# Optimization experiments

Hardware: AMD Instinct MI355X
Metric: run time of the kernel (lower is better)

Reference implementation:

```python
import jax, jax.numpy as jnp
import numpy as np

L = 2        # num_layers
H = 512      # hidden_size
IN = 32      # input_size = output_size + 24
OUT = 8      # output_size
B = 512      # batch
S = 128      # encoder seq_len
F = 48       # future_len
TF = 24      # time-feature dim


def setup_inputs() -> dict:
    key = jax.random.key(0)
    ks = jax.random.split(key, 14)
    def rn(k, shape, s=0.05):
        return jax.random.normal(k, shape, dtype=jnp.float32) * s
    return {
        "x": rn(ks[0], (S, B, IN), 1.0),
        "future_time": rn(ks[1], (F - 1, B, TF), 1.0),
        "h0": rn(ks[2], (L, 1, H), 1.0),
        "c0": rn(ks[3], (L, 1, H), 1.0),
        # PyTorch nn.LSTM weights: gate order (i, f, g, o), rows of 4H
        "w_ih0": rn(ks[4], (4 * H, IN)),
        "w_hh0": rn(ks[5], (4 * H, H)),
        "b_ih0": rn(ks[6], (4 * H,)),
        "b_hh0": rn(ks[7], (4 * H,)),
        "w_ih1": rn(ks[8], (4 * H, H)),
        "w_hh1": rn(ks[9], (4 * H, H)),
        "b_ih1": rn(ks[10], (4 * H,)),
        "b_hh1": rn(ks[11], (4 * H,)),
        "fc_w": rn(ks[12], (OUT, H)),
        "fc_b": rn(ks[13], (OUT,)),
    }


def _cell(x, h, c, w_ih, w_hh, b):
    # PyTorch LSTMCell math, gate order i,f,g,o
    gates = x @ w_ih.T + h @ w_hh.T + b  # [B, 4H]
    i, f, g, o = jnp.split(gates, 4, axis=-1)
    c2 = jax.nn.sigmoid(f) * c + jax.nn.sigmoid(i) * jnp.tanh(g)
    h2 = jax.nn.sigmoid(o) * jnp.tanh(c2)
    return h2, c2


def reference(x, future_time, h0, c0,
              w_ih0, w_hh0, b_ih0, b_hh0,
              w_ih1, w_hh1, b_ih1, b_hh1,
              fc_w, fc_b):
    batch = x.shape[1]
    params = [(w_ih0, w_hh0, b_ih0 + b_hh0),
              (w_ih1, w_hh1, b_ih1 + b_hh1)]
    h_init = jnp.broadcast_to(h0, (L, batch, H))
    c_init = jnp.broadcast_to(c0, (L, batch, H))

    def multi_step(carry, x_t):
        hs, cs = carry
        new_h, new_c = [], []
        inp = x_t
        for l, (wi, wh, b) in enumerate(params):
            h2, c2 = _cell(inp, hs[l], cs[l], wi, wh, b)
            new_h.append(h2)
            new_c.append(c2)
            inp = h2
        return (jnp.stack(new_h), jnp.stack(new_c)), inp

    # encoder pass over the conditioning sequence
    (hs, cs), outs = jax.lax.scan(multi_step, (h_init, c_init), x)
    y0 = outs[-1] @ fc_w.T + fc_b  # [B, OUT], first prediction

    def dec_step(carry, t_feat):
        hs, cs, y = carry
        x_t = jnp.concatenate([y, t_feat], axis=-1)  # [B, OUT+TF] == [B, IN]
        (hs2, cs2), h_top = multi_step((hs, cs), x_t)
        y2 = h_top @ fc_w.T + fc_b
        return (hs2, cs2, y2), y2

    _, ys = jax.lax.scan(dec_step, (hs, cs, y0), future_time)
    return jnp.concatenate([y0[None], ys], axis=0)  # [future_len, B, OUT]
```

## Files before the change

### kernel.cpp

```cpp
#include <hip/hip_runtime.h>


typedef __attribute__((ext_vector_type(8))) short bf16x8;
typedef __attribute__((ext_vector_type(16))) float f32x16;

#define MFMA32(a, b, c) __builtin_amdgcn_mfma_f32_32x32x16_bf16((a), (b), (c), 0, 0, 0)
#define DEV static __device__ __forceinline__

constexpr int kSeq = 128;
constexpr int kT = 175;
constexpr int kRB = 65536;

constexpr size_t kWsHbuf = 0;
constexpr size_t kWsYacc = 2ull * 2 * 8 * kRB;
constexpr size_t kWsFlag = kWsYacc + 2ull * 512 * 8 * 4;
constexpr size_t kWsRc   = kWsFlag + 2ull * 8 * 32 * 64;
constexpr size_t kWsEnd  = kWsRc + 2ull * 8 * 64;
constexpr size_t kWsZeroBegin = kWsYacc;
constexpr size_t kWsZeroSize  = kWsEnd - kWsYacc;

DEV unsigned short f2bf(float f) {
  unsigned u = __float_as_uint(f);
  u += 0x7fffu + ((u >> 16) & 1u);
  return (unsigned short)(u >> 16);
}
DEV float bf2f(unsigned short s) { return __uint_as_float(((unsigned)s) << 16); }
DEV float sigf(float v) { return 1.0f / (1.0f + __expf(-v)); }
DEV float tanhf_(float v) { float e = __expf(2.0f * v); return 1.0f - 2.0f / (e + 1.0f); }
DEV f32x16 zero16() {
  f32x16 z;
#pragma unroll
  for (int i = 0; i < 16; ++i) z[i] = 0.0f;
  return z;
}
DEV bf16x8 pack8(const float* p) {
  float4 a = *(const float4*)p;
  float4 b = *(const float4*)(p + 4);
  bf16x8 r;
  r[0] = (short)f2bf(a.x); r[1] = (short)f2bf(a.y);
  r[2] = (short)f2bf(a.z); r[3] = (short)f2bf(a.w);
  r[4] = (short)f2bf(b.x); r[5] = (short)f2bf(b.y);
  r[6] = (short)f2bf(b.z); r[7] = (short)f2bf(b.w);
  return r;
}

DEV unsigned ald(const unsigned* p) {
  return __hip_atomic_load(p, __ATOMIC_RELAXED, __HIP_MEMORY_SCOPE_AGENT);
}
DEV void ast(unsigned* p, unsigned v) {
  __hip_atomic_store(p, v, __ATOMIC_RELAXED, __HIP_MEMORY_SCOPE_AGENT);
}
DEV unsigned long long ald64(const unsigned long long* p) {
  return __hip_atomic_load(p, __ATOMIC_RELAXED, __HIP_MEMORY_SCOPE_AGENT);
}
DEV void ast64(unsigned long long* p, unsigned long long v) {
  __hip_atomic_store(p, v, __ATOMIC_RELAXED, __HIP_MEMORY_SCOPE_AGENT);
}
DEV float aldf(const float* p) {
  return __hip_atomic_load(p, __ATOMIC_RELAXED, __HIP_MEMORY_SCOPE_AGENT);
}
DEV void astf(float* p, float v) {
  __hip_atomic_store(p, v, __ATOMIC_RELAXED, __HIP_MEMORY_SCOPE_AGENT);
}
DEV void relwait() {
  __atomic_signal_fence(__ATOMIC_SEQ_CST);
  __builtin_amdgcn_s_waitcnt(0);
  __atomic_signal_fence(__ATOMIC_SEQ_CST);
}
DEV bool pollw(const unsigned* slot, unsigned thr) {
  for (int it = 0; it < (1 << 22); ++it) {
    const unsigned v = ald(slot);
    if (__ballot(v < thr) == 0ull) {
      __atomic_signal_fence(__ATOMIC_ACQUIRE);
      return true;
    }
    __builtin_amdgcn_s_sleep(1);
  }
  return false;
}

#define PARTS_WRITE(accv, ms_, ns_)                                           \
  { const int gate_ = (ns_)*2 + gbit;                                         \
    _Pragma("unroll") for (int rg = 0; rg < 16; ++rg) {                       \
      const int r_ = (ms_)*32 + (rg & 3) + 4 * hi5 + 8 * (rg >> 2);           \
      partsB[((kw * 4 + gate_) * 64 + r_) * 17 + l15] = f2bf((accv)[rg]);     \
    } }

__global__ __launch_bounds__(256, 2) void lstm_persist(
    const float* __restrict__ x, const float* __restrict__ ft,
    const float* __restrict__ h0in, const float* __restrict__ c0in,
    const float* __restrict__ wih0, const float* __restrict__ whh0,
    const float* __restrict__ bih0, const float* __restrict__ bhh0,
    const float* __restrict__ wih1, const float* __restrict__ whh1,
    const float* __restrict__ bih1, const float* __restrict__ bhh1,
    const float* __restrict__ fcw, const float* __restrict__ fcb,
    float* __restrict__ out, char* __restrict__ ws) {
  __shared__ __attribute__((aligned(16))) unsigned short partsB[16 * 64 * 17];
  __shared__ __attribute__((aligned(16))) unsigned short xin[64 * 40];
  __shared__ __attribute__((aligned(16))) unsigned short hloc[64 * 24];
  __shared__ float biasl[4][16];
  __shared__ float fcwl[8][16];
  __shared__ unsigned bflag;

  const int bid = blockIdx.x;
  const int layer = bid >> 8;
  const int idx = bid & 255;
  const int bc = idx & 7;
  const int hc = idx >> 3;
  const int b0 = bc * 64;
  const int u0 = hc * 16;
  const int tid = threadIdx.x;
  const int kw = tid >> 6;
  const int lane = tid & 63;
  const int l31 = lane & 31, l15 = lane & 15, hi5 = lane >> 5, gbit = (lane >> 4) & 1;

  char* hbuf = ws + kWsHbuf;
  float* yacc = (float*)(ws + kWsYacc);
  unsigned* flg = (unsigned*)(ws + kWsFlag);
  unsigned* rc = (unsigned*)(ws + kWsRc);

  auto fslot = [&](int l, int b, int h) { return flg + (((l * 8) + b) * 32 + h) * 16; };
  auto region = [&](int p, int l, int b) -> char* {
    return hbuf + (size_t)(((p * 2) + l) * 8 + b) * kRB;
  };

  bool alive = true;

  bf16x8 wf[2][16];
#pragma unroll
  for (int ns = 0; ns < 2; ++ns) {
    const int gate = ns * 2 + gbit;
    const int wrow = gate * 512 + u0 + l15;
    if (layer) {
#pragma unroll
      for (int m = 0; m < 16; ++m) {
        const int jg = kw + 4 * m;
        const int k0 = jg * 16 + hi5 * 8;
        const float* p = (k0 < 512) ? (wih1 + wrow * 512 + k0)
                                    : (whh1 + wrow * 512 + (k0 - 512));
        wf[ns][m] = pack8(p);
      }
    } else {
#pragma unroll
      for (int m = 0; m < 8; ++m) {
        const int jg = kw + 4 * m;
        wf[ns][m] = pack8(whh0 + wrow * 512 + jg * 16 + hi5 * 8);
      }
      if (kw < 2) wf[ns][8] = pack8(wih0 + wrow * 32 + kw * 16 + hi5 * 8);
    }
  }

  if (tid < 64) {
    const int g = tid >> 4, h = tid & 15;
    const int row = g * 512 + u0 + h;
    biasl[g][h] = layer ? (bih1[row] + bhh1[row]) : (bih0[row] + bhh0[row]);
  }
  if (layer && tid >= 64 && tid < 192) {
    const int t2 = tid - 64;
    fcwl[t2 >> 4][t2 & 15] = fcw[(t2 >> 4) * 512 + u0 + (t2 & 15)];
  }

  const int own_h = tid & 15;
  const int own_r0 = (tid >> 4) * 4;
  float cst[4];
  {
    const float cv = c0in[layer * 512 + u0 + own_h];
    cst[0] = cst[1] = cst[2] = cst[3] = cv;
  }

  {
    char* dst = region(layer ? 0 : 1, layer, bc);
    if (tid < 128) {
      const int r = tid >> 1, half = tid & 1;
      union { unsigned short s[8]; unsigned long long u[2]; } v;
#pragma unroll
      for (int k2 = 0; k2 < 8; ++k2)
        v.s[k2] = f2bf(h0in[layer * 512 + u0 + half * 8 + k2]);
      unsigned long long* dp =
          (unsigned long long*)(dst + ((u0 >> 3) + half) * 1024 + r * 16);
      ast64(dp, v.u[0]); ast64(dp + 1, v.u[1]);
    }
    relwait();
    __syncthreads();
    if (tid == 0) ast(fslot(layer, bc, hc), 1u);
  }

  auto xin_store = [&](int r, int c4, float4 v) {
    const int gx = c4 >> 3, half = (c4 >> 2) & 1;
    uint2 pv;
    pv.x = (unsigned)f2bf(v.x) | ((unsigned)f2bf(v.y) << 16);
    pv.y = (unsigned)f2bf(v.z) | ((unsigned)f2bf(v.w) << 16);
    *(uint2*)&xin[r * 40 + ((gx ^ (r & 3)) << 3) + half * 4] = pv;
  };

  auto cell_update = [&]() {
#pragma unroll
    for (int i = 0; i < 4; ++i) {
      const int r = own_r0 + i;
      float ig = biasl[0][own_h], fg = biasl[1][own_h];
      float gg = biasl[2][own_h], og = biasl[3][own_h];
#pragma unroll
      for (int w2 = 0; w2 < 4; ++w2) {
        ig += bf2f(partsB[((w2 * 4 + 0) * 64 + r) * 17 + own_h]);
        fg += bf2f(partsB[((w2 * 4 + 1) * 64 + r) * 17 + own_h]);
        gg += bf2f(partsB[((w2 * 4 + 2) * 64 + r) * 17 + own_h]);
        og += bf2f(partsB[((w2 * 4 + 3) * 64 + r) * 17 + own_h]);
      }
      const float cv = sigf(fg) * cst[i] + sigf(ig) * tanhf_(gg);
      cst[i] = cv;
      hloc[r * 24 + own_h] = f2bf(sigf(og) * tanhf_(cv));
    }
  };

  auto h_publish = [&](char* dst) {
    if (tid < 128) {
      const int r = tid >> 1, half = tid & 1;
      union { uint4 q; unsigned long long u[2]; } v;
      v.q = *(const uint4*)&hloc[r * 24 + half * 8];
      unsigned long long* dp =
          (unsigned long long*)(dst + ((u0 >> 3) + half) * 1024 + r * 16);
      ast64(dp, v.u[0]); ast64(dp + 1, v.u[1]);
    }
  };

  if (layer == 0) {
    for (int t = 0; t < kT; ++t) {
      if (kw == 0 && alive) {
        const unsigned* slot = (lane < 32)
            ? fslot(0, bc, lane)
            : fslot(1, bc, lane - 32);
        const unsigned thr = (lane < 32)
            ? (unsigned)(t + 1)
            : (unsigned)((t < kSeq) ? t : t + 1);
        alive = pollw(slot, thr);
      }
      __syncthreads();

      if (t < kSeq) {
#pragma unroll
        for (int it = 0; it < 2; ++it) {
          const int u = tid + it * 256;
          const int r = u >> 3, c4 = (u & 7) * 4;
          xin_store(r, c4, *(const float4*)&x[(size_t)(t * 512 + b0 + r) * 32 + c4]);
        }
        __syncthreads();
      } else {
        const int q = (t - 1) & 1;
        if (tid < 128) {
          const int r = tid >> 1, o4 = (tid & 1) * 4;
          const float* yp = &yacc[(size_t)(q * 512 + b0 + r) * 8 + o4];
          float4 v;
          v.x = aldf(yp + 0); v.y = aldf(yp + 1);
          v.z = aldf(yp + 2); v.w = aldf(yp + 3);
          const float4 bb = *(const float4*)&fcb[o4];
          v.x += bb.x; v.y += bb.y; v.z += bb.z; v.w += bb.w;
          if (hc == 0)
            *(float4*)&out[(size_t)((t - kSeq) * 512 + b0 + r) * 8 + o4] = v;
          xin_store(r, o4, v);
        }
        for (int u = tid; u < 384; u += 256) {
          const int r = u / 6, m = u - r * 6;
          xin_store(r, 8 + m * 4,
                    *(const float4*)&ft[(size_t)((t - kSeq) * 512 + b0 + r) * 24 + m * 4]);
        }
        __syncthreads();
        if (tid == 0) {
          const unsigned old = __hip_atomic_fetch_add(rc + (q * 8 + bc) * 16, 1u,
                                                      __ATOMIC_RELAXED,
                                                      __HIP_MEMORY_SCOPE_AGENT);
          bflag = (old == 31u) ? 1u : 0u;
        }
        __syncthreads();
        if (bflag) {
          for (int u = tid; u < 512; u += 256)
            astf(&yacc[(size_t)q * 512 * 8 + (size_t)b0 * 8 + u], 0.0f);
          relwait();
          __syncthreads();
          if (tid == 0) ast(rc + (q * 8 + bc) * 16, 0u);
        }
      }

      f32x16 acc00 = zero16(), acc01 = zero16(), acc10 = zero16(), acc11 = zero16();
      const char* hb0 = region((t - 1) & 1, 0, bc);
      unsigned long long abuf[2][16];
#pragma unroll
      for (int i = 0; i < 4; ++i) {
        const size_t off = (size_t)((2 * (kw + 4 * i) + hi5) * 64 + l31) * 16;
        const unsigned long long* p = (const unsigned long long*)(hb0 + off);
        abuf[0][i * 4 + 0] = ald64(p);
        abuf[0][i * 4 + 1] = ald64(p + 1);
        const unsigned long long* q2 = (const unsigned long long*)(hb0 + off + 512);
        abuf[0][i * 4 + 2] = ald64(q2);
        abuf[0][i * 4 + 3] = ald64(q2 + 1);
      }
#pragma unroll
      for (int g = 0; g < 2; ++g) {
        if (g == 0) {
#pragma unroll
          for (int i = 0; i < 4; ++i) {
            const int m = 4 + i;
            const size_t off = (size_t)((2 * (kw + 4 * m) + hi5) * 64 + l31) * 16;
            const unsigned long long* p = (const unsigned long long*)(hb0 + off);
            abuf[1][i * 4 + 0] = ald64(p);
            abuf[1][i * 4 + 1] = ald64(p + 1);
            const unsigned long long* q2 = (const unsigned long long*)(hb0 + off + 512);
            abuf[1][i * 4 + 2] = ald64(q2);
            abuf[1][i * 4 + 3] = ald64(q2 + 1);
          }
        }
#pragma unroll
        for (int i = 0; i < 4; ++i) {
          const int m = g * 4 + i;
          union { unsigned long long u[2]; bf16x8 v; } a0, a1;
          a0.u[0] = abuf[g][i * 4 + 0]; a0.u[1] = abuf[g][i * 4 + 1];
          a1.u[0] = abuf[g][i * 4 + 2]; a1.u[1] = abuf[g][i * 4 + 3];
          acc00 = MFMA32(a0.v, wf[0][m], acc00);
          acc01 = MFMA32(a0.v, wf[1][m], acc01);
          acc10 = MFMA32(a1.v, wf[0][m], acc10);
          acc11 = MFMA32(a1.v, wf[1][m], acc11);
        }
      }
      if (kw < 2) {
#pragma unroll
        for (int ms = 0; ms < 2; ++ms) {
          const int r = ms * 32 + l31;
          const int gx = kw * 2 + hi5;
          const bf16x8 a = *(const bf16x8*)&xin[r * 40 + ((gx ^ (r & 3)) << 3)];
          if (ms == 0) {
            acc00 = MFMA32(a, wf[0][8], acc00);
            acc01 = MFMA32(a, wf[1][8], acc01);
          } else {
            acc10 = MFMA32(a, wf[0][8], acc10);
            acc11 = MFMA32(a, wf[1][8], acc11);
          }
        }
      }
      PARTS_WRITE(acc00, 0, 0); PARTS_WRITE(acc01, 0, 1);
      PARTS_WRITE(acc10, 1, 0); PARTS_WRITE(acc11, 1, 1);
      __syncthreads();
      cell_update();
      __syncthreads();
      h_publish(region(t & 1, 0, bc));
      relwait();
      __syncthreads();
      if (tid == 0) ast(fslot(0, bc, hc), (unsigned)(t + 2));
    }
    if (hc == 0) {
      if (kw == 0 && alive)
        alive = pollw(fslot(1, bc, lane & 31), (unsigned)(kT + 1));
      __syncthreads();
      for (int u = tid; u < 512; u += 256) {
        const int r = u >> 3, o = u & 7;
        out[(size_t)(47 * 512 + b0 + r) * 8 + o] =
            aldf(&yacc[(size_t)(b0 + r) * 8 + o]) + fcb[o];
      }
    }
  } else {
    for (int t = 0; t < kT; ++t) {
      if (kw == 0 && alive) {
        const unsigned* slot = (lane < 32)
            ? fslot(0, bc, lane)
            : fslot(1, bc, lane - 32);
        const unsigned thr = (lane < 32) ? (unsigned)(t + 2) : (unsigned)(t + 1);
        alive = pollw(slot, thr);
      }
      __syncthreads();

      f32x16 acc00 = zero16(), acc01 = zero16(), acc10 = zero16(), acc11 = zero16();
      const char* hbA = region(t & 1, 0, bc);
      const char* hbB = region(t & 1, 1, bc);
      unsigned long long abuf[2][16];
#pragma unroll
      for (int i = 0; i < 4; ++i) {
        const char* base = hbA;
        const size_t off = (size_t)((2 * (kw + 4 * i) + hi5) * 64 + l31) * 16;
        const unsigned long long* p = (const unsigned long long*)(base + off);
        abuf[0][i * 4 + 0] = ald64(p);
        abuf[0][i * 4 + 1] = ald64(p + 1);
        const unsigned long long* q2 = (const unsigned long long*)(base + off + 512);
        abuf[0][i * 4 + 2] = ald64(q2);
        abuf[0][i * 4 + 3] = ald64(q2 + 1);
      }
#pragma unroll
      for (int g = 0; g < 4; ++g) {
        if (g < 3) {
          const int gn = g + 1;
#pragma unroll
          for (int i = 0; i < 4; ++i) {
            const int m = gn * 4 + i;
            const char* base = (m < 8) ? hbA : hbB;
            const int jl = (kw + 4 * m) & 31;
            const size_t off = (size_t)((2 * jl + hi5) * 64 + l31) * 16;
            const unsigned long long* p = (const unsigned long long*)(base + off);
            abuf[gn & 1][i * 4 + 0] = ald64(p);
            abuf[gn & 1][i * 4 + 1] = ald64(p + 1);
            const unsigned long long* q2 = (const unsigned long long*)(base + off + 512);
            abuf[gn & 1][i * 4 + 2] = ald64(q2);
            abuf[gn & 1][i * 4 + 3] = ald64(q2 + 1);
          }
        }
#pragma unroll
        for (int i = 0; i < 4; ++i) {
          const int m = g * 4 + i;
          union { unsigned long long u[2]; bf16x8 v; } a0, a1;
          a0.u[0] = abuf[g & 1][i * 4 + 0]; a0.u[1] = abuf[g & 1][i * 4 + 1];
          a1.u[0] = abuf[g & 1][i * 4 + 2]; a1.u[1] = abuf[g & 1][i * 4 + 3];
          acc00 = MFMA32(a0.v, wf[0][m], acc00);
          acc01 = MFMA32(a0.v, wf[1][m], acc01);
          acc10 = MFMA32(a1.v, wf[0][m], acc10);
          acc11 = MFMA32(a1.v, wf[1][m], acc11);
        }
      }
      PARTS_WRITE(acc00, 0, 0); PARTS_WRITE(acc01, 0, 1);
      PARTS_WRITE(acc10, 1, 0); PARTS_WRITE(acc11, 1, 1);
      __syncthreads();
      cell_update();
      __syncthreads();
      h_publish(region((t & 1) ^ 1, 1, bc));
      if (t >= kSeq - 1) {
        const int q = t & 1;
#pragma unroll
        for (int rep = 0; rep < 2; ++rep) {
          const int i2 = tid + rep * 256;
          const int r = i2 >> 3, o = i2 & 7;
          float s = 0.0f;
#pragma unroll
          for (int h2 = 0; h2 < 16; ++h2)
            s += bf2f(hloc[r * 24 + h2]) * fcwl[o][h2];
          atomicAdd(&yacc[(size_t)(q * 512 + b0 + r) * 8 + o], s);
        }
      }
      relwait();
      __syncthreads();
      if (tid == 0) ast(fslot(1, bc, hc), (unsigned)(t + 2));
    }
  }
}

extern "C" void kernel_launch(void* const* d_in, const int* in_sizes, int n_in,
                              void* d_out, int out_size, void* d_ws, size_t ws_size,
                              hipStream_t stream) {
  (void)in_sizes; (void)n_in; (void)out_size; (void)ws_size;
  hipMemsetAsync((char*)d_ws + kWsZeroBegin, 0, kWsZeroSize, stream);

  const float* x    = (const float*)d_in[0];
  const float* ft   = (const float*)d_in[1];
  const float* h0in = (const float*)d_in[2];
  const float* c0in = (const float*)d_in[3];
  const float* wih0 = (const float*)d_in[4];
  const float* whh0 = (const float*)d_in[5];
  const float* bih0 = (const float*)d_in[6];
  const float* bhh0 = (const float*)d_in[7];
  const float* wih1 = (const float*)d_in[8];
  const float* whh1 = (const float*)d_in[9];
  const float* bih1 = (const float*)d_in[10];
  const float* bhh1 = (const float*)d_in[11];
  const float* fcw  = (const float*)d_in[12];
  const float* fcb  = (const float*)d_in[13];
  float* out = (float*)d_out;
  char* ws = (char*)d_ws;

  void* args[] = {&x, &ft, &h0in, &c0in, &wih0, &whh0, &bih0, &bhh0,
                  &wih1, &whh1, &bih1, &bhh1, &fcw, &fcb, &out, &ws};
  hipError_t err = hipLaunchCooperativeKernel((void*)lstm_persist, dim3(512),
                                              dim3(256), args, 0, stream);
  if (err != hipSuccess) {
    lstm_persist<<<dim3(512), dim3(256), 0, stream>>>(
        x, ft, h0in, c0in, wih0, whh0, bih0, bhh0,
        wih1, whh1, bih1, bhh1, fcw, fcb, out, ws);
  }
}
```

Baseline: 3.383 ms.

## Compute FC output redundantly in layer-0 blocks and deepen layer-0 h buffering

Drops the atomicAdd-based FC accumulation in layer-1 blocks and the reset-counter protocol. Instead, each layer-0 block computes y = h1·fc_w^T itself with MFMA from the published layer-1 hidden state. Layer-0 h buffers go from double to quadruple buffering, which lets layer 0 run up to a few steps ahead of layer 1 during the encoder phase. Layer-1 loads are also issued three groups ahead. This removes global atomics and an extra barrier round, at the cost of every layer-0 block redundantly reading h1 and doing the small FC matmul.

```diff
diff --git a/kernel.cpp b/kernel.cpp
--- a/kernel.cpp
+++ b/kernel.cpp
@@ -11,13 +11,12 @@
 constexpr int kT = 175;
 constexpr int kRB = 65536;
 
-constexpr size_t kWsHbuf = 0;
-constexpr size_t kWsYacc = 2ull * 2 * 8 * kRB;
-constexpr size_t kWsFlag = kWsYacc + 2ull * 512 * 8 * 4;
-constexpr size_t kWsRc   = kWsFlag + 2ull * 8 * 32 * 64;
-constexpr size_t kWsEnd  = kWsRc + 2ull * 8 * 64;
-constexpr size_t kWsZeroBegin = kWsYacc;
-constexpr size_t kWsZeroSize  = kWsEnd - kWsYacc;
+constexpr size_t kWsH0   = 0;
+constexpr size_t kWsH1   = 4ull * 8 * kRB;
+constexpr size_t kWsFlag = kWsH1 + 2ull * 8 * kRB;
+constexpr size_t kWsEnd  = kWsFlag + 2ull * 8 * 32 * 64;
+constexpr size_t kWsZeroBegin = kWsFlag;
+constexpr size_t kWsZeroSize  = kWsEnd - kWsFlag;
 
 DEV unsigned short f2bf(float f) {
   unsigned u = __float_as_uint(f);
@@ -54,12 +53,6 @@
   return __hip_atomic_load(p, __ATOMIC_RELAXED, __HIP_MEMORY_SCOPE_AGENT);
 }
 DEV void ast64(unsigned long long* p, unsigned long long v) {
-  __hip_atomic_store(p, v, __ATOMIC_RELAXED, __HIP_MEMORY_SCOPE_AGENT);
-}
-DEV float aldf(const float* p) {
-  return __hip_atomic_load(p, __ATOMIC_RELAXED, __HIP_MEMORY_SCOPE_AGENT);
-}
-DEV void astf(float* p, float v) {
   __hip_atomic_store(p, v, __ATOMIC_RELAXED, __HIP_MEMORY_SCOPE_AGENT);
 }
 DEV void relwait() {
@@ -99,8 +92,6 @@
   __shared__ __attribute__((aligned(16))) unsigned short xin[64 * 40];
   __shared__ __attribute__((aligned(16))) unsigned short hloc[64 * 24];
   __shared__ float biasl[4][16];
-  __shared__ float fcwl[8][16];
-  __shared__ unsigned bflag;
 
   const int bid = blockIdx.x;
   const int layer = bid >> 8;
@@ -114,14 +105,13 @@
   const int lane = tid & 63;
   const int l31 = lane & 31, l15 = lane & 15, hi5 = lane >> 5, gbit = (lane >> 4) & 1;
 
-  char* hbuf = ws + kWsHbuf;
-  float* yacc = (float*)(ws + kWsYacc);
   unsigned* flg = (unsigned*)(ws + kWsFlag);
-  unsigned* rc = (unsigned*)(ws + kWsRc);
-
   auto fslot = [&](int l, int b, int h) { return flg + (((l * 8) + b) * 32 + h) * 16; };
-  auto region = [&](int p, int l, int b) -> char* {
-    return hbuf + (size_t)(((p * 2) + l) * 8 + b) * kRB;
+  auto region0 = [&](int d, int b) -> char* {
+    return ws + kWsH0 + (size_t)(d * 8 + b) * kRB;
+  };
+  auto region1 = [&](int p, int b) -> char* {
+    return ws + kWsH1 + (size_t)(p * 8 + b) * kRB;
   };
 
   bool alive = true;
@@ -155,10 +145,6 @@
     const int row = g * 512 + u0 + h;
     biasl[g][h] = layer ? (bih1[row] + bhh1[row]) : (bih0[row] + bhh0[row]);
   }
-  if (layer && tid >= 64 && tid < 192) {
-    const int t2 = tid - 64;
-    fcwl[t2 >> 4][t2 & 15] = fcw[(t2 >> 4) * 512 + u0 + (t2 & 15)];
-  }
 
   const int own_h = tid & 15;
   const int own_r0 = (tid >> 4) * 4;
@@ -169,7 +155,7 @@
   }
 
   {
-    char* dst = region(layer ? 0 : 1, layer, bc);
+    char* dst = layer ? region1(0, bc) : region0(3, bc);
     if (tid < 128) {
       const int r = tid >> 1, half = tid & 1;
       union { unsigned short s[8]; unsigned long long u[2]; } v;
@@ -224,6 +210,81 @@
   };
 
   if (layer == 0) {
+    bf16x8 wfc[8];
+#pragma unroll
+    for (int m = 0; m < 8; ++m) {
+      if (l31 < 8) {
+        wfc[m] = pack8(fcw + l31 * 512 + (kw + 4 * m) * 16 + hi5 * 8);
+      } else {
+#pragma unroll
+        for (int j = 0; j < 8; ++j) wfc[m][j] = (short)0;
+      }
+    }
+
+    auto y_from_h1 = [&](const char* hbY) -> float4 {
+      f32x16 ay0 = zero16(), ay1 = zero16();
+      unsigned long long ab[2][16];
+#pragma unroll
+      for (int i = 0; i < 4; ++i) {
+        const size_t off = (size_t)((2 * (kw + 4 * i) + hi5) * 64 + l31) * 16;
+        const unsigned long long* p = (const unsigned long long*)(hbY + off);
+        ab[0][i * 4 + 0] = ald64(p);
+        ab[0][i * 4 + 1] = ald64(p + 1);
+        const unsigned long long* q2 = (const unsigned long long*)(hbY + off + 512);
+        ab[0][i * 4 + 2] = ald64(q2);
+        ab[0][i * 4 + 3] = ald64(q2 + 1);
+      }
+#pragma unroll
+      for (int g = 0; g < 2; ++g) {
+        if (g == 0) {
+#pragma unroll
+          for (int i = 0; i < 4; ++i) {
+            const int m = 4 + i;
+            const size_t off = (size_t)((2 * (kw + 4 * m) + hi5) * 64 + l31) * 16;
+            const unsigned long long* p = (const unsigned long long*)(hbY + off);
+            ab[1][i * 4 + 0] = ald64(p);
+            ab[1][i * 4 + 1] = ald64(p + 1);
+            const unsigned long long* q2 = (const unsigned long long*)(hbY + off + 512);
+            ab[1][i * 4 + 2] = ald64(q2);
+            ab[1][i * 4 + 3] = ald64(q2 + 1);
+          }
+        }
+#pragma unroll
+        for (int i = 0; i < 4; ++i) {
+          const int m = g * 4 + i;
+          union { unsigned long long u[2]; bf16x8 v; } a0, a1;
+          a0.u[0] = ab[g][i * 4 + 0]; a0.u[1] = ab[g][i * 4 + 1];
+          a1.u[0] = ab[g][i * 4 + 2]; a1.u[1] = ab[g][i * 4 + 3];
+          ay0 = MFMA32(a0.v, wfc[m], ay0);
+          ay1 = MFMA32(a1.v, wfc[m], ay1);
+        }
+      }
+      float* ypr = (float*)partsB;
+      if (l31 < 8) {
+#pragma unroll
+        for (int rg = 0; rg < 16; ++rg) {
+          const int row = (rg & 3) + 8 * (rg >> 2) + 4 * hi5;
+          ypr[(kw * 64 + row) * 8 + l31] = ay0[rg];
+          ypr[(kw * 64 + 32 + row) * 8 + l31] = ay1[rg];
+        }
+      }
+      __syncthreads();
+      float4 v = {0.f, 0.f, 0.f, 0.f};
+      if (tid < 128) {
+        const int r = tid >> 1, o4 = (tid & 1) * 4;
+#pragma unroll
+        for (int w2 = 0; w2 < 4; ++w2) {
+          v.x += ypr[(w2 * 64 + r) * 8 + o4 + 0];
+          v.y += ypr[(w2 * 64 + r) * 8 + o4 + 1];
+          v.z += ypr[(w2 * 64 + r) * 8 + o4 + 2];
+          v.w += ypr[(w2 * 64 + r) * 8 + o4 + 3];
+        }
+        const float4 bb = *(const float4*)&fcb[o4];
+        v.x += bb.x; v.y += bb.y; v.z += bb.z; v.w += bb.w;
+      }
+      return v;
+    };
+
     for (int t = 0; t < kT; ++t) {
       if (kw == 0 && alive) {
         const unsigned* slot = (lane < 32)
@@ -231,7 +292,7 @@
             : fslot(1, bc, lane - 32);
         const unsigned thr = (lane < 32)
             ? (unsigned)(t + 1)
-            : (unsigned)((t < kSeq) ? t : t + 1);
+            : (unsigned)((t < kSeq) ? (t >= 3 ? t - 2 : 0) : (t + 1));
         alive = pollw(slot, thr);
       }
       __syncthreads();
@@ -245,15 +306,9 @@
         }
         __syncthreads();
       } else {
-        const int q = (t - 1) & 1;
+        const float4 v = y_from_h1(region1(t & 1, bc));
         if (tid < 128) {
           const int r = tid >> 1, o4 = (tid & 1) * 4;
-          const float* yp = &yacc[(size_t)(q * 512 + b0 + r) * 8 + o4];
-          float4 v;
-          v.x = aldf(yp + 0); v.y = aldf(yp + 1);
-          v.z = aldf(yp + 2); v.w = aldf(yp + 3);
-          const float4 bb = *(const float4*)&fcb[o4];
-          v.x += bb.x; v.y += bb.y; v.z += bb.z; v.w += bb.w;
           if (hc == 0)
             *(float4*)&out[(size_t)((t - kSeq) * 512 + b0 + r) * 8 + o4] = v;
           xin_store(r, o4, v);
@@ -264,24 +319,10 @@
                     *(const float4*)&ft[(size_t)((t - kSeq) * 512 + b0 + r) * 24 + m * 4]);
         }
         __syncthreads();
-        if (tid == 0) {
-          const unsigned old = __hip_atomic_fetch_add(rc + (q * 8 + bc) * 16, 1u,
-                                                      __ATOMIC_RELAXED,
-                                                      __HIP_MEMORY_SCOPE_AGENT);
-          bflag = (old == 31u) ? 1u : 0u;
-        }
-        __syncthreads();
-        if (bflag) {
-          for (int u = tid; u < 512; u += 256)
-            astf(&yacc[(size_t)q * 512 * 8 + (size_t)b0 * 8 + u], 0.0f);
-          relwait();
-          __syncthreads();
-          if (tid == 0) ast(rc + (q * 8 + bc) * 16, 0u);
-        }
       }
 
       f32x16 acc00 = zero16(), acc01 = zero16(), acc10 = zero16(), acc11 = zero16();
-      const char* hb0 = region((t - 1) & 1, 0, bc);
+      const char* hb0 = region0((t + 3) & 3, bc);
       unsigned long long abuf[2][16];
 #pragma unroll
       for (int i = 0; i < 4; ++i) {
@@ -340,7 +381,7 @@
       __syncthreads();
       cell_update();
       __syncthreads();
-      h_publish(region(t & 1, 0, bc));
+      h_publish(region0(t & 3, bc));
       relwait();
       __syncthreads();
       if (tid == 0) ast(fslot(0, bc, hc), (unsigned)(t + 2));
@@ -349,10 +390,10 @@
       if (kw == 0 && alive)
         alive = pollw(fslot(1, bc, lane & 31), (unsigned)(kT + 1));
       __syncthreads();
-      for (int u = tid; u < 512; u += 256) {
-        const int r = u >> 3, o = u & 7;
-        out[(size_t)(47 * 512 + b0 + r) * 8 + o] =
-            aldf(&yacc[(size_t)(b0 + r) * 8 + o]) + fcb[o];
+      const float4 v = y_from_h1(region1(kT & 1, bc));
+      if (tid < 128) {
+        const int r = tid >> 1, o4 = (tid & 1) * 4;
+        *(float4*)&out[(size_t)(47 * 512 + b0 + r) * 8 + o4] = v;
       }
     }
   } else {
@@ -367,69 +408,49 @@
       __syncthreads();
 
       f32x16 acc00 = zero16(), acc01 = zero16(), acc10 = zero16(), acc11 = zero16();
-      const char* hbA = region(t & 1, 0, bc);
-      const char* hbB = region(t & 1, 1, bc);
-      unsigned long long abuf[2][16];
-#pragma unroll
-      for (int i = 0; i < 4; ++i) {
-        const char* base = hbA;
-        const size_t off = (size_t)((2 * (kw + 4 * i) + hi5) * 64 + l31) * 16;
-        const unsigned long long* p = (const unsigned long long*)(base + off);
-        abuf[0][i * 4 + 0] = ald64(p);
-        abuf[0][i * 4 + 1] = ald64(p + 1);
-        const unsigned long long* q2 = (const unsigned long long*)(base + off + 512);
-        abuf[0][i * 4 + 2] = ald64(q2);
-        abuf[0][i * 4 + 3] = ald64(q2 + 1);
-      }
-#pragma unroll
-      for (int g = 0; g < 4; ++g) {
-        if (g < 3) {
-          const int gn = g + 1;
-#pragma unroll
-          for (int i = 0; i < 4; ++i) {
-            const int m = gn * 4 + i;
-            const char* base = (m < 8) ? hbA : hbB;
-            const int jl = (kw + 4 * m) & 31;
-            const size_t off = (size_t)((2 * jl + hi5) * 64 + l31) * 16;
-            const unsigned long long* p = (const unsigned long long*)(base + off);
-            abuf[gn & 1][i * 4 + 0] = ald64(p);
-            abuf[gn & 1][i * 4 + 1] = ald64(p + 1);
-            const unsigned long long* q2 = (const unsigned long long*)(base + off + 512);
-            abuf[gn & 1][i * 4 + 2] = ald64(q2);
-            abuf[gn & 1][i * 4 + 3] = ald64(q2 + 1);
-          }
-        }
+      const char* hbA = region0(t & 3, bc);
+      const char* hbB = region1(t & 1, bc);
+      unsigned long long ab0[16], ab1[16], ab2[16];
+      auto issue1 = [&](unsigned long long* dst, int g) {
+#pragma unroll
+        for (int i = 0; i < 4; ++i) {
+          const int m = g * 4 + i;
+          const char* base = (m < 8) ? hbA : hbB;
+          const int jl = (kw + 4 * m) & 31;
+          const size_t off = (size_t)((2 * jl + hi5) * 64 + l31) * 16;
+          const unsigned long long* p = (const unsigned long long*)(base + off);
+          dst[i * 4 + 0] = ald64(p);
+          dst[i * 4 + 1] = ald64(p + 1);
+          const unsigned long long* q2 = (const unsigned long long*)(base + off + 512);
+          dst[i * 4 + 2] = ald64(q2);
+          dst[i * 4 + 3] = ald64(q2 + 1);
+        }
+      };
+      auto compg1 = [&](const unsigned long long* src, int g) {
 #pragma unroll
         for (int i = 0; i < 4; ++i) {
           const int m = g * 4 + i;
           union { unsigned long long u[2]; bf16x8 v; } a0, a1;
-          a0.u[0] = abuf[g & 1][i * 4 + 0]; a0.u[1] = abuf[g & 1][i * 4 + 1];
-          a1.u[0] = abuf[g & 1][i * 4 + 2]; a1.u[1] = abuf[g & 1][i * 4 + 3];
+          a0.u[0] = src[i * 4 + 0]; a0.u[1] = src[i * 4 + 1];
+          a1.u[0] = src[i * 4 + 2]; a1.u[1] = src[i * 4 + 3];
           acc00 = MFMA32(a0.v, wf[0][m], acc00);
           acc01 = MFMA32(a0.v, wf[1][m], acc01);
           acc10 = MFMA32(a1.v, wf[0][m], acc10);
           acc11 = MFMA32(a1.v, wf[1][m], acc11);
         }
-      }
+      };
+      issue1(ab0, 0); issue1(ab1, 1); issue1(ab2, 2);
+      compg1(ab0, 0);
+      issue1(ab0, 3);
+      compg1(ab1, 1);
+      compg1(ab2, 2);
+      compg1(ab0, 3);
       PARTS_WRITE(acc00, 0, 0); PARTS_WRITE(acc01, 0, 1);
       PARTS_WRITE(acc10, 1, 0); PARTS_WRITE(acc11, 1, 1);
       __syncthreads();
       cell_update();
       __syncthreads();
-      h_publish(region((t & 1) ^ 1, 1, bc));
-      if (t >= kSeq - 1) {
-        const int q = t & 1;
-#pragma unroll
-        for (int rep = 0; rep < 2; ++rep) {
-          const int i2 = tid + rep * 256;
-          const int r = i2 >> 3, o = i2 & 7;
-          float s = 0.0f;
-#pragma unroll
-          for (int h2 = 0; h2 < 16; ++h2)
-            s += bf2f(hloc[r * 24 + h2]) * fcwl[o][h2];
-          atomicAdd(&yacc[(size_t)(q * 512 + b0 + r) * 8 + o], s);
-        }
-      }
+      h_publish(region1((t & 1) ^ 1, bc));
       relwait();
       __syncthreads();
       if (tid == 0) ast(fslot(1, bc, hc), (unsigned)(t + 2));
```

After: 6.811 ms. 101% more time.
